# Optimization experiments

Measured on AMD Instinct MI355X. Metric: run time of the kernel, lower is better.

Reference implementation:

```python
import jax, jax.numpy as jnp
import numpy as np

B, T, I, H = 64, 512, 128, 2048
SPARSITY = 0.1
SPECTRAL_RADIUS = 0.95


def setup_inputs() -> dict:
    key = jax.random.key(0)
    kx, kin = jax.random.split(key)
    x = jax.random.normal(kx, (B, T, I), dtype=jnp.float32)
    W_in = jax.random.normal(kin, (H, I), dtype=jnp.float32)
    # Build reservoir matrix like the torch module: randn, zeroed where rand < sparsity,
    # then scaled to the target spectral radius.
    rng = np.random.default_rng(0)
    W_res = rng.standard_normal((H, H)).astype(np.float32)
    mask = rng.random((H, H)) < SPARSITY
    W_res = np.where(mask, 0.0, W_res)
    radius = np.max(np.abs(np.linalg.eigvals(W_res))).real
    W_res = (W_res * (SPECTRAL_RADIUS / radius)).astype(np.float32)
    return {"x": x, "W_in": W_in, "W_res": jnp.asarray(W_res)}


def reference(x, W_in, W_res):
    # h_t = tanh(W_in @ x_t^T + W_res @ h_{t-1}^T)^T, expressed batch-major.
    b, t, _ = x.shape
    h0 = jnp.zeros((b, W_res.shape[0]), dtype=x.dtype)

    def step(h, xt):  # h: [B,H], xt: [B,I]
        h_new = jnp.tanh(xt @ W_in.T + h @ W_res.T)
        return h_new, None

    x_tbi = jnp.swapaxes(x, 0, 1)  # [T,B,I]
    h_final, _ = jax.lax.scan(step, h0, x_tbi)
    return h_final  # [B,H]
```

## Files before the change

### kernel.cpp

```cpp
#include <hip/hip_runtime.h>


#define B_ 64
#define T_ 512
#define I_ 128
#define H_ 2048
#define NWG 256
#define ROWS 32
#define BATS 16
#define WPAD 2056
#define IPAD 136
#define PPAD 33
#define FSTRIDE 16

typedef _Float16 f16;
typedef f16 f16x8 __attribute__((ext_vector_type(8)));
typedef float f32x4 __attribute__((ext_vector_type(4)));
typedef unsigned long long u64;
typedef unsigned int u32;
typedef unsigned short u16;
typedef u32 u32x4 __attribute__((ext_vector_type(4)));

#define TAG32 0x00010001u

#define LDS_WRES   0
#define LDS_WINHI  131584
#define LDS_WINLO  (131584 + 8704)
#define LDS_PART   (131584 + 17408)
#define LDS_TOTAL  (131584 + 17408 + 8448)

extern "C" __global__ __launch_bounds__(256, 1)
void esn_kernel(const float* __restrict__ x, const float* __restrict__ Win,
                const float* __restrict__ Wres, float* __restrict__ out,
                u16* ht0, u16* ht1, int* flags)
{
    extern __shared__ char lds[];
    f16*   Wr   = (f16*)(lds + LDS_WRES);
    f16*   Whi  = (f16*)(lds + LDS_WINHI);
    f16*   Wlo  = (f16*)(lds + LDS_WINLO);
    float* part = (float*)(lds + LDS_PART);

    const int tid  = threadIdx.x;
    const int wg   = blockIdx.x;
    const int bg   = (wg & 7) >> 1;
    const int j    = ((wg >> 3) << 1) | (wg & 1);
    const int lid  = (bg << 6) | j;
    const bool leader = (wg < 8);
    const int r0   = j * ROWS;
    const int b0   = bg * BATS;
    const int wv   = tid >> 6;
    const int lane = tid & 63;
    const int lm   = lane & 15;
    const int quad = lane >> 4;

    for (int idx = tid; idx < ROWS * (H_ / 4); idx += 256) {
        int r  = idx >> 9;
        int c4 = idx & 511;
        const float4 v = ((const float4*)(Wres + (size_t)(r0 + r) * H_))[c4];
        f16* dst = Wr + r * WPAD + c4 * 4;
        dst[0] = (f16)v.x; dst[1] = (f16)v.y; dst[2] = (f16)v.z; dst[3] = (f16)v.w;
    }
    for (int idx = tid; idx < ROWS * (I_ / 4); idx += 256) {
        int r  = idx >> 5;
        int c4 = idx & 31;
        const float4 v = ((const float4*)(Win + (size_t)(r0 + r) * I_))[c4];
        float vv[4] = {v.x, v.y, v.z, v.w};
        f16* dh = Whi + r * IPAD + c4 * 4;
        f16* dl = Wlo + r * IPAD + c4 * 4;
        #pragma unroll
        for (int q = 0; q < 4; q++) {
            f16 hi = (f16)vv[q];
            dh[q] = hi;
            dl[q] = (f16)(vv[q] - (float)hi);
        }
    }
    __syncthreads();

    for (int t = 0; t < T_; t++) {
        const u16* hrd = (t & 1) ? ht1 : ht0;
        u16*       hwr = (t & 1) ? ht0 : ht1;
        const u32  E32 = ((t >> 1) & 1) ? TAG32 : 0u;

        f32x4 acc0 = {0.f, 0.f, 0.f, 0.f};
        f32x4 acc1 = {0.f, 0.f, 0.f, 0.f};

        {
            const int kin = wv * 32 + quad * 8;
            const float* xp = x + ((size_t)(b0 + lm) * T_ + t) * I_ + kin;
            float xf[8];
            *(float4*)(xf)     = *(const float4*)(xp);
            *(float4*)(xf + 4) = *(const float4*)(xp + 4);
            f16x8 xhi, xlo;
            #pragma unroll
            for (int qq = 0; qq < 8; qq++) {
                f16 hi = (f16)xf[qq];
                xhi[qq] = hi;
                xlo[qq] = (f16)(xf[qq] - (float)hi);
            }
            f16x8 bh0 = *(const f16x8*)(Whi + lm * IPAD + kin);
            f16x8 bh1 = *(const f16x8*)(Whi + (lm + 16) * IPAD + kin);
            f16x8 bl0 = *(const f16x8*)(Wlo + lm * IPAD + kin);
            f16x8 bl1 = *(const f16x8*)(Wlo + (lm + 16) * IPAD + kin);
            acc0 = __builtin_amdgcn_mfma_f32_16x16x32_f16(xhi, bh0, acc0, 0, 0, 0);
            acc1 = __builtin_amdgcn_mfma_f32_16x16x32_f16(xhi, bh1, acc1, 0, 0, 0);
            acc0 = __builtin_amdgcn_mfma_f32_16x16x32_f16(xlo, bh0, acc0, 0, 0, 0);
            acc1 = __builtin_amdgcn_mfma_f32_16x16x32_f16(xlo, bh1, acc1, 0, 0, 0);
            acc0 = __builtin_amdgcn_mfma_f32_16x16x32_f16(xhi, bl0, acc0, 0, 0, 0);
            acc1 = __builtin_amdgcn_mfma_f32_16x16x32_f16(xhi, bl1, acc1, 0, 0, 0);
        }

        {
            const int* fp = flags + ((t & 1) * NWG + (bg << 6) + (wv << 4)
                                     + (lane & 15)) * FSTRIDE;
            int spins = 0;
            for (;;) {
                int f = __hip_atomic_load(fp, __ATOMIC_RELAXED,
                                          __HIP_MEMORY_SCOPE_AGENT);
                if (__all(f >= t)) break;
                if (++spins > 4096) break;
                __builtin_amdgcn_s_sleep(1);
            }
        }

        if (leader) __builtin_amdgcn_fence(__ATOMIC_ACQUIRE, "agent");

        const u64 hb = (u64)hrd + ((u64)(b0 + lm) << 12) + (wv << 10) + (quad << 4);

        u32x4 v[16];
        #pragma unroll
        for (int ks = 0; ks < 16; ks++) {
            asm volatile("global_load_dwordx4 %0, %1, off sc0"
                         : "=&v"(v[ks]) : "v"(hb + (u64)(ks * 64)));
        }
        asm volatile("s_waitcnt vmcnt(0)" ::: "memory");

        int rounds = 0;
        for (;;) {
            u32 bad = 0;
            #pragma unroll
            for (int ks = 0; ks < 16; ks++)
                #pragma unroll
                for (int e = 0; e < 4; e++)
                    bad |= (v[ks][e] & TAG32) ^ E32;
            if (__all(bad == 0)) break;
            ++rounds;
            if (leader) __builtin_amdgcn_fence(__ATOMIC_ACQUIRE, "agent");
            if (bad) {
                __builtin_amdgcn_s_sleep(1);
                if (rounds < 8) {
                    #pragma unroll
                    for (int ks = 0; ks < 16; ks++) {
                        asm volatile("global_load_dwordx4 %0, %1, off sc0"
                                     : "=&v"(v[ks]) : "v"(hb + (u64)(ks * 64)));
                    }
                } else {
                    #pragma unroll
                    for (int ks = 0; ks < 16; ks++) {
                        asm volatile("global_load_dwordx4 %0, %1, off sc0 sc1"
                                     : "=&v"(v[ks]) : "v"(hb + (u64)(ks * 64)));
                    }
                }
            }
            asm volatile("s_waitcnt vmcnt(0)" ::: "memory");
        }

        {
            const f16* w0 = Wr + lm * WPAD + wv * 512 + quad * 8;
            const f16* w1 = Wr + (lm + 16) * WPAD + wv * 512 + quad * 8;
            #pragma unroll
            for (int ks = 0; ks < 16; ks++) {
                f16x8 af;
                #pragma unroll
                for (int e = 0; e < 4; e++)
                    ((u32*)&af)[e] = v[ks][e] & ~TAG32;
                f16x8 bf0 = *(const f16x8*)(w0 + ks * 32);
                f16x8 bf1 = *(const f16x8*)(w1 + ks * 32);
                acc0 = __builtin_amdgcn_mfma_f32_16x16x32_f16(af, bf0, acc0, 0, 0, 0);
                acc1 = __builtin_amdgcn_mfma_f32_16x16x32_f16(af, bf1, acc1, 0, 0, 0);
            }
        }

        {
            float* pw = part + wv * (BATS * PPAD);
            #pragma unroll
            for (int r = 0; r < 4; r++) {
                int m = quad * 4 + r;
                pw[m * PPAD + lm]      = acc0[r];
                pw[m * PPAD + 16 + lm] = acc1[r];
            }
        }
        __syncthreads();

        if (t == T_ - 1) {
            const int m = tid >> 4;
            const int n = (tid & 15) * 2;
            const int o = m * PPAD + n;
            float s0 = part[o]     + part[BATS * PPAD + o]     + part[2 * BATS * PPAD + o]
                     + part[3 * BATS * PPAD + o];
            float s1 = part[o + 1] + part[BATS * PPAD + o + 1] + part[2 * BATS * PPAD + o + 1]
                     + part[3 * BATS * PPAD + o + 1];
            float* op = out + (size_t)(b0 + m) * H_ + r0 + n;
            op[0] = tanhf(s0);
            op[1] = tanhf(s1);
        } else if (tid < 128) {
            const int m  = tid >> 3;
            const int n0 = (tid & 7) * 4;
            const u16 bit = (u16)(((t + 1) >> 1) & 1);
            union { u16 h[4]; u64 u; } pk;
            #pragma unroll
            for (int e = 0; e < 4; e++) {
                const int o = m * PPAD + n0 + e;
                float s = part[o] + part[BATS * PPAD + o] + part[2 * BATS * PPAD + o]
                        + part[3 * BATS * PPAD + o];
                union { f16 f; u16 u; } cv;
                cv.f = (f16)tanhf(s);
                pk.h[e] = (u16)((cv.u & 0xFFFEu) | bit);
            }
            __hip_atomic_store((u64*)(hwr + (size_t)(b0 + m) * H_ + r0 + n0),
                               pk.u, __ATOMIC_RELAXED, __HIP_MEMORY_SCOPE_AGENT);
        }

        __syncthreads();

        if (t < T_ - 1 && tid == 0) {
            __hip_atomic_store(flags + (((t + 1) & 1) * NWG + lid) * FSTRIDE,
                               t + 1, __ATOMIC_RELAXED, __HIP_MEMORY_SCOPE_AGENT);
        }
    }
}

extern "C" void kernel_launch(void* const* d_in, const int* in_sizes, int n_in,
                              void* d_out, int out_size, void* d_ws, size_t ws_size,
                              hipStream_t stream)
{
    (void)in_sizes; (void)n_in; (void)out_size; (void)ws_size;
    const float* x    = (const float*)d_in[0];
    const float* Win  = (const float*)d_in[1];
    const float* Wres = (const float*)d_in[2];
    float* out = (float*)d_out;

    u16* ht0 = (u16*)d_ws;
    u16* ht1 = ht0 + (size_t)B_ * H_;
    int* flags = (int*)((char*)d_ws + (size_t)2 * B_ * H_ * sizeof(u16));

    hipMemsetAsync(d_ws, 0x00, (size_t)B_ * H_ * sizeof(u16), stream);
    hipMemsetAsync((char*)d_ws + (size_t)B_ * H_ * sizeof(u16), 0x01,
                   (size_t)B_ * H_ * sizeof(u16), stream);
    hipMemsetAsync(flags, 0, (size_t)2 * NWG * FSTRIDE * sizeof(int), stream);

    hipFuncSetAttribute((const void*)esn_kernel,
                        hipFuncAttributeMaxDynamicSharedMemorySize, LDS_TOTAL);

    void* args[] = {(void*)&x, (void*)&Win, (void*)&Wres, (void*)&out,
                    (void*)&ht0, (void*)&ht1, (void*)&flags};
    hipLaunchCooperativeKernel((const void*)esn_kernel, dim3(NWG), dim3(256),
                               args, LDS_TOTAL, stream);
}
```

Before: 2.591 ms.

## Consume hidden-state chunks incrementally as their producer flags become ready

The kernel used to wait until all 16 producer flags for the wave were set, then load the whole hidden-state slice and do the recurrent MFMAs. Now it polls the flags as a ballot mask, loads and validates only the chunks whose producers are ready, and runs their MFMAs right away, looping until every chunk is consumed. This overlaps recurrent compute with producers that finish late, so the per-step critical path is shorter. In exchange it adds per-chunk branching, more polling iterations and serialized waitcnts, which may cost latency when all producers finish at about the same time.

New measurement: 3.083 ms. 1.19x slower.

```diff
diff --git a/kernel.cpp b/kernel.cpp
--- a/kernel.cpp
+++ b/kernel.cpp
@@ -109,66 +109,49 @@
             acc1 = __builtin_amdgcn_mfma_f32_16x16x32_f16(xhi, bl1, acc1, 0, 0, 0);
         }
 
-        {
-            const int* fp = flags + ((t & 1) * NWG + (bg << 6) + (wv << 4)
-                                     + (lane & 15)) * FSTRIDE;
-            int spins = 0;
-            for (;;) {
-                int f = __hip_atomic_load(fp, __ATOMIC_RELAXED,
-                                          __HIP_MEMORY_SCOPE_AGENT);
-                if (__all(f >= t)) break;
-                if (++spins > 4096) break;
-                __builtin_amdgcn_s_sleep(1);
-            }
-        }
-
-        if (leader) __builtin_amdgcn_fence(__ATOMIC_ACQUIRE, "agent");
-
         const u64 hb = (u64)hrd + ((u64)(b0 + lm) << 12) + (wv << 10) + (quad << 4);
+        const f16* w0 = Wr + lm * WPAD + wv * 512 + quad * 8;
+        const f16* w1 = Wr + (lm + 16) * WPAD + wv * 512 + quad * 8;
+        const int* fp = flags + ((t & 1) * NWG + (bg << 6) + (wv << 4)
+                                 + (lane & 15)) * FSTRIDE;
 
         u32x4 v[16];
-        #pragma unroll
-        for (int ks = 0; ks < 16; ks++) {
-            asm volatile("global_load_dwordx4 %0, %1, off sc0"
-                         : "=&v"(v[ks]) : "v"(hb + (u64)(ks * 64)));
-        }
-        asm volatile("s_waitcnt vmcnt(0)" ::: "memory");
-
-        int rounds = 0;
-        for (;;) {
-            u32 bad = 0;
+        u32 pend = 0xFFFFu;
+        int spins = 0;
+        while (pend) {
+            if (leader) __builtin_amdgcn_fence(__ATOMIC_ACQUIRE, "agent");
+            int f = __hip_atomic_load(fp, __ATOMIC_RELAXED,
+                                      __HIP_MEMORY_SCOPE_AGENT);
+            u32 ready = (u32)__ballot(f >= t) & 0xFFFFu;
+            u32 go = ready & pend;
+            if (++spins > 4096) go = pend;
+            if (!go) { __builtin_amdgcn_s_sleep(1); continue; }
+
             #pragma unroll
             for (int ks = 0; ks < 16; ks++)
-                #pragma unroll
-                for (int e = 0; e < 4; e++)
-                    bad |= (v[ks][e] & TAG32) ^ E32;
-            if (__all(bad == 0)) break;
-            ++rounds;
-            if (leader) __builtin_amdgcn_fence(__ATOMIC_ACQUIRE, "agent");
-            if (bad) {
-                __builtin_amdgcn_s_sleep(1);
-                if (rounds < 8) {
-                    #pragma unroll
-                    for (int ks = 0; ks < 16; ks++) {
+                if (go & (1u << ks))
+                    asm volatile("global_load_dwordx4 %0, %1, off sc0"
+                                 : "=&v"(v[ks]) : "v"(hb + (u64)(ks * 64)));
+            asm volatile("s_waitcnt vmcnt(0)" ::: "memory");
+
+            #pragma unroll
+            for (int ks = 0; ks < 16; ks++) {
+                if (!(go & (1u << ks))) continue;
+                int rounds = 0;
+                for (;;) {
+                    u32 bad = ((v[ks][0] & TAG32) ^ E32) | ((v[ks][1] & TAG32) ^ E32)
+                            | ((v[ks][2] & TAG32) ^ E32) | ((v[ks][3] & TAG32) ^ E32);
+                    if (__all(bad == 0)) break;
+                    __builtin_amdgcn_s_sleep(1);
+                    if (++rounds < 4) {
                         asm volatile("global_load_dwordx4 %0, %1, off sc0"
                                      : "=&v"(v[ks]) : "v"(hb + (u64)(ks * 64)));
-                    }
-                } else {
-                    #pragma unroll
-                    for (int ks = 0; ks < 16; ks++) {
+                    } else {
                         asm volatile("global_load_dwordx4 %0, %1, off sc0 sc1"
                                      : "=&v"(v[ks]) : "v"(hb + (u64)(ks * 64)));
                     }
+                    asm volatile("s_waitcnt vmcnt(0)" ::: "memory");
                 }
-            }
-            asm volatile("s_waitcnt vmcnt(0)" ::: "memory");
-        }
-
-        {
-            const f16* w0 = Wr + lm * WPAD + wv * 512 + quad * 8;
-            const f16* w1 = Wr + (lm + 16) * WPAD + wv * 512 + quad * 8;
-            #pragma unroll
-            for (int ks = 0; ks < 16; ks++) {
                 f16x8 af;
                 #pragma unroll
                 for (int e = 0; e < 4; e++)
@@ -178,6 +161,7 @@
                 acc0 = __builtin_amdgcn_mfma_f32_16x16x32_f16(af, bf0, acc0, 0, 0, 0);
                 acc1 = __builtin_amdgcn_mfma_f32_16x16x32_f16(af, bf1, acc1, 0, 0, 0);
             }
+            pend &= ~go;
         }
 
         {
```
